# Kernel optimization log

Measured on AMD Instinct MI355X. Metric: run time of the kernel, lower is better.

Reference implementation:

```python
import jax, jax.numpy as jnp
import numpy as np
import math

B, C, DH = 2048, 64, 512
CAP_VOCAB = 11  # max(core_capacities)+1
DIST_VOCAB = 3


def setup_inputs() -> dict:
    key = jax.random.key(0)
    ks = jax.random.split(key, 12)
    inp = {
        "Ht_C": jax.random.normal(ks[0], (B, C, DH), jnp.float32),
        "core_capacities": jax.random.randint(ks[1], (B, C), 0, CAP_VOCAB),
        "distances": jax.random.randint(ks[2], (B, C), 0, DIST_VOCAB),
        "H_X": jax.random.normal(ks[3], (B, DH), jnp.float32),
        "Ht_S": jax.random.normal(ks[4], (B, DH), jnp.float32),
        "Eq_Q": jax.random.normal(ks[5], (B, DH), jnp.float32),
        "double": jax.random.randint(ks[6], (B,), 0, 2).astype(bool),
        # learned parameters (nn.Embedding tables and bias-free Linear weights, [out,in])
        "cap_emb": jax.random.normal(ks[7], (CAP_VOCAB, DH), jnp.float32) * 0.02,
        "dist_emb": jax.random.normal(ks[8], (DIST_VOCAB, DH), jnp.float32) * 0.02,
        "W_q": jax.random.normal(ks[9], (DH, 3 * DH), jnp.float32) * (1.0 / math.sqrt(3 * DH)),
        "W_k": jax.random.normal(ks[10], (DH, DH), jnp.float32) * (1.0 / math.sqrt(DH)),
        "W_v": jax.random.normal(ks[11], (DH, DH), jnp.float32) * (1.0 / math.sqrt(DH)),
    }
    return inp


def reference(Ht_C, core_capacities, distances, H_X, Ht_S, Eq_Q, double,
              cap_emb, dist_emb, W_q, W_k, W_v):
    scale = 1.0 / math.sqrt(Ht_C.shape[-1])  # 1/sqrt(d_H), slice_emb_size == d_H
    # dynamic core embeddings G_{t,q}^{(C)}: [B,C,dH]
    G = Ht_C + cap_emb[core_capacities] + dist_emb[distances]
    # context and projections
    context = jnp.concatenate([H_X, Ht_S, Eq_Q], axis=-1)          # [B,3dH]
    Q = context @ W_q.T                                            # [B,dH]
    K = jnp.einsum('bcd,ed->bce', G, W_k)                          # [B,C,dH]
    V = jnp.einsum('bcd,ed->bce', G, W_v)                          # [B,C,dH]
    # glimpse attention over cores
    attn_logits = jnp.einsum('bcd,bd->bc', K, Q) * scale           # [B,C]
    attn_weights = jax.nn.softmax(attn_logits, axis=-1)            # softmax over cores
    glimpse = jnp.einsum('bc,bcd->bd', attn_weights, V)            # [B,dH]
    # pointer logits + capacity mask
    u = jnp.einsum('bcd,bd->bc', K, glimpse) * scale               # [B,C]
    need = jnp.where(double[:, None], 2, 1)                        # [B,1]
    invalid = core_capacities < need                               # [B,C]
    u = jnp.where(invalid, -jnp.inf, u)
    return jax.nn.softmax(u, axis=-1)                              # [B,C]
```

## Files before the change

kernel.cpp:

```cpp
#include <hip/hip_runtime.h>
#include <math.h>

#define DH 512
#define CC 64
#define NB 2048
#define SCALE 0.044194173824159216f

#define PD(d) ((((d) >> 5) * 36) + ((d) & 31))

__device__ __forceinline__ float wsum(float v) {
#pragma unroll
  for (int off = 32; off; off >>= 1) v += __shfl_xor(v, off, 64);
  return v;
}

__global__ __launch_bounds__(128) void pre_kernel(const float* __restrict__ Wq,
                                                  const float* __restrict__ Wv,
                                                  const float* __restrict__ Wk,
                                                  float* __restrict__ Aout,
                                                  float* __restrict__ Mout,
                                                  const unsigned char* __restrict__ dbl,
                                                  int* __restrict__ need) {
  const int bx = blockIdx.x;
  const int t = threadIdx.x;
  if (bx == 256) {
    __shared__ int flagNZ, flagFP;
    if (t == 0) { flagNZ = 0; flagFP = 0; }
    __syncthreads();
    int nz = 0, fp = 0;
    for (int i = t; i < NB; i += 128) {
      if (i & 3) {
        unsigned char v = dbl[i];
        nz |= (v != 0);
        fp |= (v == 0x3f) | (v == 0x80);
      }
    }
    if (nz) atomicOr(&flagNZ, 1);
    if (fp) atomicOr(&flagFP, 1);
    __syncthreads();
    const int isFP = flagFP, isByte = flagNZ && !flagFP;
    for (int i = t; i < NB; i += 128) {
      int v;
      if (isFP)        v = (((const float*)dbl)[i] != 0.0f);
      else if (isByte) v = (dbl[i] != 0);
      else             v = (((const int*)dbl)[i] != 0);
      need[i] = v ? 2 : 1;
    }
    return;
  }
  __shared__ float As[16][64];
  __shared__ float Bs[16][64];
  const int mt = bx >> 3, nt = bx & 7;
  const int m0 = mt * 64, n0 = nt * 64;
  const bool isQ = (m0 < 1536);
  const float* Acol = isQ ? (Wq + m0) : (Wv + (m0 - 1536));
  const int lda = isQ ? 1536 : 512;
  float* Cout = isQ ? (Aout + (size_t)m0 * 512) : (Mout + (size_t)(m0 - 1536) * 512);
  const int lr = t >> 3;
  const int lc = (t & 7) << 3;
  const int tx = t & 15, ty = t >> 4;

  float4 ra0, ra1, rb0, rb1;
  ra0 = *(const float4*)&Acol[(size_t)lr * lda + lc];
  ra1 = *(const float4*)&Acol[(size_t)lr * lda + lc + 4];
  rb0 = *(const float4*)&Wk[(size_t)lr * 512 + n0 + lc];
  rb1 = *(const float4*)&Wk[(size_t)lr * 512 + n0 + lc + 4];
  float acc[8][4] = {};
  for (int k0 = 0; k0 < 512; k0 += 16) {
    __syncthreads();
    *(float4*)&As[lr][lc] = ra0;
    *(float4*)&As[lr][lc + 4] = ra1;
    *(float4*)&Bs[lr][lc] = rb0;
    *(float4*)&Bs[lr][lc + 4] = rb1;
    __syncthreads();
    if (k0 + 16 < 512) {
      const int kn = k0 + 16 + lr;
      ra0 = *(const float4*)&Acol[(size_t)kn * lda + lc];
      ra1 = *(const float4*)&Acol[(size_t)kn * lda + lc + 4];
      rb0 = *(const float4*)&Wk[(size_t)kn * 512 + n0 + lc];
      rb1 = *(const float4*)&Wk[(size_t)kn * 512 + n0 + lc + 4];
    }
#pragma unroll
    for (int k = 0; k < 16; ++k) {
      float4 a0 = *(float4*)&As[k][ty << 3];
      float4 a1 = *(float4*)&As[k][(ty << 3) + 4];
      float4 b  = *(float4*)&Bs[k][tx << 2];
      float av[8] = {a0.x, a0.y, a0.z, a0.w, a1.x, a1.y, a1.z, a1.w};
      float bv[4] = {b.x, b.y, b.z, b.w};
#pragma unroll
      for (int i = 0; i < 8; ++i)
#pragma unroll
        for (int j = 0; j < 4; ++j) acc[i][j] = fmaf(av[i], bv[j], acc[i][j]);
    }
  }
#pragma unroll
  for (int i = 0; i < 8; ++i) {
    float4 o = {acc[i][0], acc[i][1], acc[i][2], acc[i][3]};
    *(float4*)&Cout[(size_t)((ty << 3) + i) * 512 + n0 + (tx << 2)] = o;
  }
}

#define AS_STR 132

__global__ __launch_bounds__(256) void gemm_nn2p(const float* __restrict__ A0,
                                                 const float* __restrict__ A1,
                                                 const float* __restrict__ A2,
                                                 const float* __restrict__ B,
                                                 float* __restrict__ Cp,
                                                 int kchunk) {
  __shared__ float As[16 * AS_STR];
  __shared__ float Bs[16 * 64];
  const int t = threadIdx.x;
  const int m0 = blockIdx.x * 128, n0 = blockIdx.y * 64;
  const int kbeg = blockIdx.z * kchunk, kend = kbeg + kchunk;
  float* C = Cp + (size_t)blockIdx.z * (NB * DH);
  const int tx = t & 15, ty = t >> 4;
  const int ar0 = t >> 2;
  const int ak4 = (t & 3) << 2;
  const int bk = t >> 4, bn4 = (t & 15) << 2;

  float4 ra0, ra1, rb;
  {
    const float* base = (kbeg < 512) ? A0 : ((kbeg < 1024) ? A1 : A2);
    const int kk = kbeg & 511;
    ra0 = *(const float4*)&base[(size_t)(m0 + ar0) * 512 + kk + ak4];
    ra1 = *(const float4*)&base[(size_t)(m0 + ar0 + 64) * 512 + kk + ak4];
    rb  = *(const float4*)&B[(size_t)(kbeg + bk) * 512 + n0 + bn4];
  }
  float acc[8][4] = {};
  for (int k0 = kbeg; k0 < kend; k0 += 16) {
    __syncthreads();
    As[(ak4 + 0) * AS_STR + ar0] = ra0.x;
    As[(ak4 + 1) * AS_STR + ar0] = ra0.y;
    As[(ak4 + 2) * AS_STR + ar0] = ra0.z;
    As[(ak4 + 3) * AS_STR + ar0] = ra0.w;
    As[(ak4 + 0) * AS_STR + ar0 + 64] = ra1.x;
    As[(ak4 + 1) * AS_STR + ar0 + 64] = ra1.y;
    As[(ak4 + 2) * AS_STR + ar0 + 64] = ra1.z;
    As[(ak4 + 3) * AS_STR + ar0 + 64] = ra1.w;
    *(float4*)&Bs[bk * 64 + bn4] = rb;
    __syncthreads();
    if (k0 + 16 < kend) {
      const int kn = k0 + 16;
      const float* base = (kn < 512) ? A0 : ((kn < 1024) ? A1 : A2);
      const int kk = kn & 511;
      ra0 = *(const float4*)&base[(size_t)(m0 + ar0) * 512 + kk + ak4];
      ra1 = *(const float4*)&base[(size_t)(m0 + ar0 + 64) * 512 + kk + ak4];
      rb  = *(const float4*)&B[(size_t)(kn + bk) * 512 + n0 + bn4];
    }
#pragma unroll
    for (int k = 0; k < 16; ++k) {
      float4 a0 = *(float4*)&As[k * AS_STR + (ty << 3)];
      float4 a1 = *(float4*)&As[k * AS_STR + (ty << 3) + 4];
      float4 b  = *(float4*)&Bs[k * 64 + (tx << 2)];
      float av[8] = {a0.x, a0.y, a0.z, a0.w, a1.x, a1.y, a1.z, a1.w};
      float bv[4] = {b.x, b.y, b.z, b.w};
#pragma unroll
      for (int i = 0; i < 8; ++i)
#pragma unroll
        for (int j = 0; j < 4; ++j) acc[i][j] = fmaf(av[i], bv[j], acc[i][j]);
    }
  }
#pragma unroll
  for (int i = 0; i < 8; ++i) {
    float4 o = {acc[i][0], acc[i][1], acc[i][2], acc[i][3]};
    *(float4*)&C[(size_t)(m0 + (ty << 3) + i) * 512 + n0 + (tx << 2)] = o;
  }
}

__global__ __launch_bounds__(256, 4) void fused_kernel(const float* __restrict__ HtC,
                                                       const int* __restrict__ caps,
                                                       const int* __restrict__ dists,
                                                       const float* __restrict__ Qkp,
                                                       const float* __restrict__ Mm,
                                                       const float* __restrict__ cap_emb,
                                                       const float* __restrict__ dist_emb,
                                                       const int* __restrict__ need,
                                                       float* __restrict__ out) {
  const int t = threadIdx.x;
  const int wv = t >> 6, ln = t & 63;
  const int g = ln >> 4, l16 = ln & 15;
  const int b0 = blockIdx.x << 1;

  __shared__ float qk[2][576];
  __shared__ float gks[2][576];
  __shared__ float accs[4][576];
  __shared__ float Gws[2][DH];
  __shared__ float gkp[2][2][DH];
  __shared__ float ec[CC];
  __shared__ float capQ[2][11], distQ[2][3];
  __shared__ float capE[11], distE[3];
  __shared__ float capG[2][11], distG[2][3];
  __shared__ float lsum_s;
  __shared__ int capsS[2][CC], distsS[2][CC];

  if (t < 128) {
    int hh = t >> 6, c = t & 63;
    capsS[hh][c] = caps[(size_t)(b0 + hh) * CC + c];
    distsS[hh][c] = dists[(size_t)(b0 + hh) * CC + c];
  }

#pragma unroll
  for (int h = 0; h < 2; ++h) {
    const size_t bo = (size_t)(b0 + h) * DH;
    float q0 = 0.f, q1 = 0.f;
#pragma unroll
    for (int z = 0; z < 4; ++z) {
      q0 += Qkp[(size_t)z * NB * DH + bo + t];
      q1 += Qkp[(size_t)z * NB * DH + bo + 256 + t];
    }
    qk[h][PD(t)] = q0;
    qk[h][PD(t + 256)] = q1;
  }
  __syncthreads();

#pragma unroll
  for (int h = 0; h < 2; ++h) {
#pragma unroll
    for (int r = 0; r < 3; ++r) {
      int v = wv + (r << 2);
      if (v < 11) {
        float s = 0.f;
#pragma unroll
        for (int j = 0; j < 8; ++j)
          s = fmaf(cap_emb[v * DH + ln + (j << 6)], qk[h][PD(ln + (j << 6))], s);
        s = wsum(s);
        if (ln == 0) capQ[h][v] = s;
      }
    }
    if (wv < 3) {
      float s = 0.f;
#pragma unroll
      for (int j = 0; j < 8; ++j)
        s = fmaf(dist_emb[wv * DH + ln + (j << 6)], qk[h][PD(ln + (j << 6))], s);
      s = wsum(s);
      if (ln == 0) distQ[h][wv] = s;
    }
  }

  for (int h = 0; h < 2; ++h) {
    const int b = b0 + h;
    if (t < 11) capE[t] = 0.f;
    if (t < 3) distE[t] = 0.f;
    __syncthreads();
    float4 qs[8];
#pragma unroll
    for (int j = 0; j < 8; ++j) qs[j] = *(const float4*)&qk[h][l16 * 36 + 4 * j];
    float4 ac[8];
#pragma unroll
    for (int j = 0; j < 8; ++j) ac[j] = make_float4(0.f, 0.f, 0.f, 0.f);
    const float* hb = HtC + (size_t)b * CC * DH;
#pragma unroll 1
    for (int k = 0; k < 4; ++k) {
      const int c = (wv << 4) + (k << 2) + g;
      const float* hp = hb + (size_t)c * DH + (l16 << 5);
      float4 hv[8];
#pragma unroll
      for (int j = 0; j < 8; ++j) hv[j] = *(const float4*)&hp[4 * j];
      float s = 0.f;
#pragma unroll
      for (int j = 0; j < 8; ++j) {
        s = fmaf(hv[j].x, qs[j].x, s); s = fmaf(hv[j].y, qs[j].y, s);
        s = fmaf(hv[j].z, qs[j].z, s); s = fmaf(hv[j].w, qs[j].w, s);
      }
      s += __shfl_xor(s, 1, 64);
      s += __shfl_xor(s, 2, 64);
      s += __shfl_xor(s, 4, 64);
      s += __shfl_xor(s, 8, 64);
      float e = __expf(SCALE * (s + capQ[h][capsS[h][c]] + distQ[h][distsS[h][c]]));
      if (l16 == 0) ec[c] = e;
#pragma unroll
      for (int j = 0; j < 8; ++j) {
        ac[j].x = fmaf(e, hv[j].x, ac[j].x); ac[j].y = fmaf(e, hv[j].y, ac[j].y);
        ac[j].z = fmaf(e, hv[j].z, ac[j].z); ac[j].w = fmaf(e, hv[j].w, ac[j].w);
      }
    }
#pragma unroll
    for (int j = 0; j < 8; ++j) {
      ac[j].x += __shfl_xor(ac[j].x, 16, 64); ac[j].x += __shfl_xor(ac[j].x, 32, 64);
      ac[j].y += __shfl_xor(ac[j].y, 16, 64); ac[j].y += __shfl_xor(ac[j].y, 32, 64);
      ac[j].z += __shfl_xor(ac[j].z, 16, 64); ac[j].z += __shfl_xor(ac[j].z, 32, 64);
      ac[j].w += __shfl_xor(ac[j].w, 16, 64); ac[j].w += __shfl_xor(ac[j].w, 32, 64);
    }
    if (g == 0) {
#pragma unroll
      for (int j = 0; j < 8; ++j)
        *(float4*)&accs[wv][l16 * 36 + 4 * j] = ac[j];
    }
    __syncthreads();
    if (t < CC) {
      float e = ec[t];
      float l = wsum(e);
      if (t == 0) lsum_s = l;
      atomicAdd(&capE[capsS[h][t]], e);
      atomicAdd(&distE[distsS[h][t]], e);
    }
    __syncthreads();
    const float rinv = 1.0f / lsum_s;
#pragma unroll
    for (int dd = 0; dd < 2; ++dd) {
      int d = t + (dd << 8);
      float gg = accs[0][PD(d)] + accs[1][PD(d)] + accs[2][PD(d)] + accs[3][PD(d)];
#pragma unroll
      for (int v = 0; v < 11; ++v) gg = fmaf(capE[v], cap_emb[v * DH + d], gg);
#pragma unroll
      for (int v = 0; v < 3; ++v) gg = fmaf(distE[v], dist_emb[v * DH + d], gg);
      Gws[h][d] = gg * rinv;
    }
    __syncthreads();
  }

  {
    const int e4 = (t & 127) << 2;
    const int half = t >> 7;
    const float* Mp = Mm + (size_t)(half << 8) * DH + e4;
    const float* g0p = &Gws[0][half << 8];
    const float* g1p = &Gws[1][half << 8];
    float s00 = 0.f, s01 = 0.f, s02 = 0.f, s03 = 0.f;
    float s10 = 0.f, s11 = 0.f, s12 = 0.f, s13 = 0.f;
#pragma unroll 8
    for (int d = 0; d < 256; ++d) {
      float4 m4 = *(const float4*)&Mp[(size_t)d * DH];
      float g0 = g0p[d];
      float g1 = g1p[d];
      s00 = fmaf(g0, m4.x, s00); s01 = fmaf(g0, m4.y, s01);
      s02 = fmaf(g0, m4.z, s02); s03 = fmaf(g0, m4.w, s03);
      s10 = fmaf(g1, m4.x, s10); s11 = fmaf(g1, m4.y, s11);
      s12 = fmaf(g1, m4.z, s12); s13 = fmaf(g1, m4.w, s13);
    }
    gkp[half][0][e4 + 0] = s00; gkp[half][0][e4 + 1] = s01;
    gkp[half][0][e4 + 2] = s02; gkp[half][0][e4 + 3] = s03;
    gkp[half][1][e4 + 0] = s10; gkp[half][1][e4 + 1] = s11;
    gkp[half][1][e4 + 2] = s12; gkp[half][1][e4 + 3] = s13;
  }
  __syncthreads();
#pragma unroll
  for (int h = 0; h < 2; ++h) {
    gks[h][PD(t)] = gkp[0][h][t] + gkp[1][h][t];
    gks[h][PD(t + 256)] = gkp[0][h][t + 256] + gkp[1][h][t + 256];
  }
  __syncthreads();

#pragma unroll
  for (int h = 0; h < 2; ++h) {
#pragma unroll
    for (int r = 0; r < 3; ++r) {
      int v = wv + (r << 2);
      if (v < 11) {
        float s = 0.f;
#pragma unroll
        for (int j = 0; j < 8; ++j)
          s = fmaf(cap_emb[v * DH + ln + (j << 6)], gks[h][PD(ln + (j << 6))], s);
        s = wsum(s);
        if (ln == 0) capG[h][v] = s;
      }
    }
    if (wv < 3) {
      float s = 0.f;
#pragma unroll
      for (int j = 0; j < 8; ++j)
        s = fmaf(dist_emb[wv * DH + ln + (j << 6)], gks[h][PD(ln + (j << 6))], s);
      s = wsum(s);
      if (ln == 0) distG[h][wv] = s;
    }
  }
  __syncthreads();

  for (int h = 1; h >= 0; --h) {
    const int b = b0 + h;
    float4 gs[8];
#pragma unroll
    for (int j = 0; j < 8; ++j) gs[j] = *(const float4*)&gks[h][l16 * 36 + 4 * j];
    const float* hb = HtC + (size_t)b * CC * DH;
#pragma unroll 1
    for (int k = 0; k < 4; ++k) {
      const int c = (wv << 4) + (k << 2) + g;
      const float* hp = hb + (size_t)c * DH + (l16 << 5);
      float4 hv[8];
#pragma unroll
      for (int j = 0; j < 8; ++j) hv[j] = *(const float4*)&hp[4 * j];
      float s = 0.f;
#pragma unroll
      for (int j = 0; j < 8; ++j) {
        s = fmaf(hv[j].x, gs[j].x, s); s = fmaf(hv[j].y, gs[j].y, s);
        s = fmaf(hv[j].z, gs[j].z, s); s = fmaf(hv[j].w, gs[j].w, s);
      }
      s += __shfl_xor(s, 1, 64);
      s += __shfl_xor(s, 2, 64);
      s += __shfl_xor(s, 4, 64);
      s += __shfl_xor(s, 8, 64);
      if (l16 == 0)
        ec[c] = SCALE * (s + capG[h][capsS[h][c]] + distG[h][distsS[h][c]]);
    }
    __syncthreads();
    if (t < CC) {
      int nb = need[b];
      float x = ec[t];
      if (capsS[h][t] < nb) x = -INFINITY;
      float m = x;
#pragma unroll
      for (int off = 32; off; off >>= 1) m = fmaxf(m, __shfl_xor(m, off, 64));
      float e = __expf(x - m);
      float ssum = wsum(e);
      out[(size_t)b * CC + t] = e / ssum;
    }
    __syncthreads();
  }
}

extern "C" void kernel_launch(void* const* d_in, const int* in_sizes, int n_in,
                              void* d_out, int out_size, void* d_ws, size_t ws_size,
                              hipStream_t stream) {
  const float* HtC      = (const float*)d_in[0];
  const int* caps       = (const int*)d_in[1];
  const int* dists      = (const int*)d_in[2];
  const float* H_X      = (const float*)d_in[3];
  const float* Ht_S     = (const float*)d_in[4];
  const float* Eq_Q     = (const float*)d_in[5];
  const unsigned char* dbl = (const unsigned char*)d_in[6];
  const float* cap_emb  = (const float*)d_in[7];
  const float* dist_emb = (const float*)d_in[8];
  const float* W_q      = (const float*)d_in[9];
  const float* W_k      = (const float*)d_in[10];
  const float* W_v      = (const float*)d_in[11];
  float* out = (float*)d_out;

  float* ws     = (float*)d_ws;
  float* wsA    = ws;
  float* wsM    = wsA + 1536 * 512;
  float* wsQkp  = wsM + 512 * 512;
  int* wsNeed   = (int*)(wsQkp + 4 * 2048 * 512);

  pre_kernel<<<257, 128, 0, stream>>>(W_q, W_v, W_k, wsA, wsM, dbl, wsNeed);
  gemm_nn2p<<<dim3(16, 8, 4), 256, 0, stream>>>(H_X, Ht_S, Eq_Q, wsA, wsQkp, 384);
  fused_kernel<<<NB / 2, 256, 0, stream>>>(HtC, caps, dists, wsQkp, wsM,
                                           cap_emb, dist_emb, wsNeed, out);
}
```

Baseline: 553.9 us.

## Process four batch rows per block and prefetch HtC rows in register double buffer

The fused kernel now handles four batch rows per block instead of two, so each float4 of the M matrix read in the G·M projection is reused across four rows, halving M traffic per row. HtC row loads in both attention passes are software-pipelined with a next-iteration register buffer to hide global latency. Qkp reduction is vectorized with float4 loads. The cost is higher register and LDS use (occupancy hint relaxed to 2 waves/EU) and half as many blocks in the grid.

```diff
diff --git a/kernel.cpp b/kernel.cpp
--- a/kernel.cpp
+++ b/kernel.cpp
@@ -168,54 +168,60 @@
   }
 }
 
-__global__ __launch_bounds__(256, 4) void fused_kernel(const float* __restrict__ HtC,
-                                                       const int* __restrict__ caps,
-                                                       const int* __restrict__ dists,
-                                                       const float* __restrict__ Qkp,
-                                                       const float* __restrict__ Mm,
-                                                       const float* __restrict__ cap_emb,
-                                                       const float* __restrict__ dist_emb,
-                                                       const int* __restrict__ need,
-                                                       float* __restrict__ out) {
+__global__ __launch_bounds__(256)
+__attribute__((amdgpu_waves_per_eu(2)))
+void fused_kernel(const float* __restrict__ HtC,
+                  const int* __restrict__ caps,
+                  const int* __restrict__ dists,
+                  const float* __restrict__ Qkp,
+                  const float* __restrict__ Mm,
+                  const float* __restrict__ cap_emb,
+                  const float* __restrict__ dist_emb,
+                  const int* __restrict__ need,
+                  float* __restrict__ out) {
   const int t = threadIdx.x;
   const int wv = t >> 6, ln = t & 63;
   const int g = ln >> 4, l16 = ln & 15;
-  const int b0 = blockIdx.x << 1;
-
-  __shared__ float qk[2][576];
-  __shared__ float gks[2][576];
-  __shared__ float accs[4][576];
-  __shared__ float Gws[2][DH];
-  __shared__ float gkp[2][2][DH];
+  const int b0 = blockIdx.x << 2;
+
+  __shared__ __align__(16) float qk[4][576];
+  __shared__ __align__(16) float gks[4][576];
+  __shared__ __align__(16) float accs[4][576];
+  __shared__ __align__(16) float Gws[4][DH];
+  __shared__ __align__(16) float gkp[2][4][DH];
   __shared__ float ec[CC];
-  __shared__ float capQ[2][11], distQ[2][3];
+  __shared__ float capQ[4][11], distQ[4][3];
   __shared__ float capE[11], distE[3];
-  __shared__ float capG[2][11], distG[2][3];
+  __shared__ float capG[4][11], distG[4][3];
   __shared__ float lsum_s;
-  __shared__ int capsS[2][CC], distsS[2][CC];
-
-  if (t < 128) {
-    int hh = t >> 6, c = t & 63;
+  __shared__ int capsS[4][CC], distsS[4][CC];
+
+  {
+    const int hh = t >> 6, c = t & 63;
     capsS[hh][c] = caps[(size_t)(b0 + hh) * CC + c];
     distsS[hh][c] = dists[(size_t)(b0 + hh) * CC + c];
   }
 
-#pragma unroll
-  for (int h = 0; h < 2; ++h) {
-    const size_t bo = (size_t)(b0 + h) * DH;
-    float q0 = 0.f, q1 = 0.f;
+  {
+    const int hh = t >> 6;
+    const int d0 = (t & 63) << 3;
+    const size_t bo = (size_t)(b0 + hh) * DH + d0;
+    float4 q0 = make_float4(0.f, 0.f, 0.f, 0.f);
+    float4 q1 = make_float4(0.f, 0.f, 0.f, 0.f);
 #pragma unroll
     for (int z = 0; z < 4; ++z) {
-      q0 += Qkp[(size_t)z * NB * DH + bo + t];
-      q1 += Qkp[(size_t)z * NB * DH + bo + 256 + t];
-    }
-    qk[h][PD(t)] = q0;
-    qk[h][PD(t + 256)] = q1;
+      float4 a = *(const float4*)&Qkp[(size_t)z * NB * DH + bo];
+      float4 b4 = *(const float4*)&Qkp[(size_t)z * NB * DH + bo + 4];
+      q0.x += a.x; q0.y += a.y; q0.z += a.z; q0.w += a.w;
+      q1.x += b4.x; q1.y += b4.y; q1.z += b4.z; q1.w += b4.w;
+    }
+    *(float4*)&qk[hh][PD(d0)] = q0;
+    *(float4*)&qk[hh][PD(d0 + 4)] = q1;
   }
   __syncthreads();
 
 #pragma unroll
-  for (int h = 0; h < 2; ++h) {
+  for (int h = 0; h < 4; ++h) {
 #pragma unroll
     for (int r = 0; r < 3; ++r) {
       int v = wv + (r << 2);
@@ -238,7 +244,9 @@
     }
   }
 
-  for (int h = 0; h < 2; ++h) {
+  const int coff = l16 << 5;
+
+  for (int h = 0; h < 4; ++h) {
     const int b = b0 + h;
     if (t < 11) capE[t] = 0.f;
     if (t < 3) distE[t] = 0.f;
@@ -250,13 +258,21 @@
 #pragma unroll
     for (int j = 0; j < 8; ++j) ac[j] = make_float4(0.f, 0.f, 0.f, 0.f);
     const float* hb = HtC + (size_t)b * CC * DH;
+    float4 hv[8];
+    {
+      const float* hp = hb + (size_t)((wv << 4) + g) * DH + coff;
+#pragma unroll
+      for (int j = 0; j < 8; ++j) hv[j] = *(const float4*)&hp[4 * j];
+    }
 #pragma unroll 1
     for (int k = 0; k < 4; ++k) {
       const int c = (wv << 4) + (k << 2) + g;
-      const float* hp = hb + (size_t)c * DH + (l16 << 5);
-      float4 hv[8];
-#pragma unroll
-      for (int j = 0; j < 8; ++j) hv[j] = *(const float4*)&hp[4 * j];
+      float4 hvn[8];
+      if (k < 3) {
+        const float* hp = hb + (size_t)(c + 4) * DH + coff;
+#pragma unroll
+        for (int j = 0; j < 8; ++j) hvn[j] = *(const float4*)&hp[4 * j];
+      }
       float s = 0.f;
 #pragma unroll
       for (int j = 0; j < 8; ++j) {
@@ -274,6 +290,10 @@
         ac[j].x = fmaf(e, hv[j].x, ac[j].x); ac[j].y = fmaf(e, hv[j].y, ac[j].y);
         ac[j].z = fmaf(e, hv[j].z, ac[j].z); ac[j].w = fmaf(e, hv[j].w, ac[j].w);
       }
+      if (k < 3) {
+#pragma unroll
+        for (int j = 0; j < 8; ++j) hv[j] = hvn[j];
+      }
     }
 #pragma unroll
     for (int j = 0; j < 8; ++j) {
@@ -314,35 +334,40 @@
     const int e4 = (t & 127) << 2;
     const int half = t >> 7;
     const float* Mp = Mm + (size_t)(half << 8) * DH + e4;
-    const float* g0p = &Gws[0][half << 8];
-    const float* g1p = &Gws[1][half << 8];
-    float s00 = 0.f, s01 = 0.f, s02 = 0.f, s03 = 0.f;
-    float s10 = 0.f, s11 = 0.f, s12 = 0.f, s13 = 0.f;
-#pragma unroll 8
+    const float* gw0 = &Gws[0][half << 8];
+    const float* gw1 = &Gws[1][half << 8];
+    const float* gw2 = &Gws[2][half << 8];
+    const float* gw3 = &Gws[3][half << 8];
+    float4 s0 = make_float4(0.f, 0.f, 0.f, 0.f);
+    float4 s1 = s0, s2 = s0, s3 = s0;
+#pragma unroll 4
     for (int d = 0; d < 256; ++d) {
       float4 m4 = *(const float4*)&Mp[(size_t)d * DH];
-      float g0 = g0p[d];
-      float g1 = g1p[d];
-      s00 = fmaf(g0, m4.x, s00); s01 = fmaf(g0, m4.y, s01);
-      s02 = fmaf(g0, m4.z, s02); s03 = fmaf(g0, m4.w, s03);
-      s10 = fmaf(g1, m4.x, s10); s11 = fmaf(g1, m4.y, s11);
-      s12 = fmaf(g1, m4.z, s12); s13 = fmaf(g1, m4.w, s13);
-    }
-    gkp[half][0][e4 + 0] = s00; gkp[half][0][e4 + 1] = s01;
-    gkp[half][0][e4 + 2] = s02; gkp[half][0][e4 + 3] = s03;
-    gkp[half][1][e4 + 0] = s10; gkp[half][1][e4 + 1] = s11;
-    gkp[half][1][e4 + 2] = s12; gkp[half][1][e4 + 3] = s13;
+      float g0 = gw0[d], g1 = gw1[d], g2 = gw2[d], g3 = gw3[d];
+      s0.x = fmaf(g0, m4.x, s0.x); s0.y = fmaf(g0, m4.y, s0.y);
+      s0.z = fmaf(g0, m4.z, s0.z); s0.w = fmaf(g0, m4.w, s0.w);
+      s1.x = fmaf(g1, m4.x, s1.x); s1.y = fmaf(g1, m4.y, s1.y);
+      s1.z = fmaf(g1, m4.z, s1.z); s1.w = fmaf(g1, m4.w, s1.w);
+      s2.x = fmaf(g2, m4.x, s2.x); s2.y = fmaf(g2, m4.y, s2.y);
+      s2.z = fmaf(g2, m4.z, s2.z); s2.w = fmaf(g2, m4.w, s2.w);
+      s3.x = fmaf(g3, m4.x, s3.x); s3.y = fmaf(g3, m4.y, s3.y);
+      s3.z = fmaf(g3, m4.z, s3.z); s3.w = fmaf(g3, m4.w, s3.w);
+    }
+    *(float4*)&gkp[half][0][e4] = s0;
+    *(float4*)&gkp[half][1][e4] = s1;
+    *(float4*)&gkp[half][2][e4] = s2;
+    *(float4*)&gkp[half][3][e4] = s3;
   }
   __syncthreads();
 #pragma unroll
-  for (int h = 0; h < 2; ++h) {
+  for (int h = 0; h < 4; ++h) {
     gks[h][PD(t)] = gkp[0][h][t] + gkp[1][h][t];
     gks[h][PD(t + 256)] = gkp[0][h][t + 256] + gkp[1][h][t + 256];
   }
   __syncthreads();
 
 #pragma unroll
-  for (int h = 0; h < 2; ++h) {
+  for (int h = 0; h < 4; ++h) {
 #pragma unroll
     for (int r = 0; r < 3; ++r) {
       int v = wv + (r << 2);
@@ -366,19 +391,27 @@
   }
   __syncthreads();
 
-  for (int h = 1; h >= 0; --h) {
+  for (int h = 3; h >= 0; --h) {
     const int b = b0 + h;
     float4 gs[8];
 #pragma unroll
     for (int j = 0; j < 8; ++j) gs[j] = *(const float4*)&gks[h][l16 * 36 + 4 * j];
     const float* hb = HtC + (size_t)b * CC * DH;
+    float4 hv[8];
+    {
+      const float* hp = hb + (size_t)((wv << 4) + g) * DH + coff;
+#pragma unroll
+      for (int j = 0; j < 8; ++j) hv[j] = *(const float4*)&hp[4 * j];
+    }
 #pragma unroll 1
     for (int k = 0; k < 4; ++k) {
       const int c = (wv << 4) + (k << 2) + g;
-      const float* hp = hb + (size_t)c * DH + (l16 << 5);
-      float4 hv[8];
-#pragma unroll
-      for (int j = 0; j < 8; ++j) hv[j] = *(const float4*)&hp[4 * j];
+      float4 hvn[8];
+      if (k < 3) {
+        const float* hp = hb + (size_t)(c + 4) * DH + coff;
+#pragma unroll
+        for (int j = 0; j < 8; ++j) hvn[j] = *(const float4*)&hp[4 * j];
+      }
       float s = 0.f;
 #pragma unroll
       for (int j = 0; j < 8; ++j) {
@@ -391,6 +424,10 @@
       s += __shfl_xor(s, 8, 64);
       if (l16 == 0)
         ec[c] = SCALE * (s + capG[h][capsS[h][c]] + distG[h][distsS[h][c]]);
+      if (k < 3) {
+#pragma unroll
+        for (int j = 0; j < 8; ++j) hv[j] = hvn[j];
+      }
     }
     __syncthreads();
     if (t < CC) {
@@ -433,6 +470,6 @@
 
   pre_kernel<<<257, 128, 0, stream>>>(W_q, W_v, W_k, wsA, wsM, dbl, wsNeed);
   gemm_nn2p<<<dim3(16, 8, 4), 256, 0, stream>>>(H_X, Ht_S, Eq_Q, wsA, wsQkp, 384);
-  fused_kernel<<<NB / 2, 256, 0, stream>>>(HtC, caps, dists, wsQkp, wsM,
+  fused_kernel<<<NB / 4, 256, 0, stream>>>(HtC, caps, dists, wsQkp, wsM,
                                            cap_emb, dist_emb, wsNeed, out);
 }
```

After: 534.1 us. 3.6% less time.
